# Kernel optimization log

Hardware: AMD Instinct MI355X
Metric: run time of the kernel (lower is better)

The kernel has to match this reference:

```python
import jax, jax.numpy as jnp
import numpy as np
from jax import lax

EPS = 1e-5
SLOPE = 0.2

def knn_idx(x, k):
    # x: [B, C, N] -> neighbor indices [B, N, k] (largest negative sq-dist, self included)
    inner = jnp.einsum('bcn,bcm->bnm', x, x)          # [B,N,N]
    xx = jnp.sum(x * x, axis=1)                        # [B,N]
    pair = 2.0 * inner - xx[:, :, None] - xx[:, None, :]
    return lax.top_k(pair, k)[1]                       # [B,N,k]

def graph_feature(x, idx):
    # x: [B,C,N], idx: [B,N,k] -> edge features [B,N,k,2C] = (x_j - x_i, x_i)
    feat = jnp.transpose(x, (0, 2, 1))                 # [B,N,C]
    nbr = jax.vmap(lambda f, i: f[i])(feat, idx)       # [B,N,k,C]
    ctr = jnp.broadcast_to(feat[:, :, None, :], nbr.shape)
    return jnp.concatenate([nbr - ctr, ctr], axis=-1)  # [B,N,k,2C]

def bn(x, gamma, beta, axes):
    mu = jnp.mean(x, axis=axes, keepdims=True)
    var = jnp.var(x, axis=axes, keepdims=True)
    return (x - mu) * lax.rsqrt(var + EPS) * gamma + beta

def edge_conv(e, w, gamma, beta):
    # e: [B,N,k,2C], w: [O,2C] (1x1 conv, no bias) -> [B,N,O] after BN+LeakyReLU+max over k
    h = jnp.einsum('bnkc,oc->bnko', e, w)
    h = jax.nn.leaky_relu(bn(h, gamma, beta, (0, 1, 2)), SLOPE)
    return jnp.max(h, axis=2)                          # [B,N,O]

def setup_inputs() -> dict:
    key = jax.random.key(0)
    ks = jax.random.split(key, 8)
    B, C, N, O = 8, 3, 4096, 64
    x = jax.random.normal(ks[0], (B, C, N), jnp.float32)
    w_s = jax.random.normal(ks[1], (O, 2 * C), jnp.float32) * (1.0 / np.sqrt(2 * C))
    w_l = jax.random.normal(ks[2], (O, 2 * C), jnp.float32) * (1.0 / np.sqrt(2 * C))
    w_f = jax.random.normal(ks[3], (O, 2 * O), jnp.float32) * (1.0 / np.sqrt(2 * O))
    g_s = jnp.ones((O,)); b_s = jnp.zeros((O,))
    g_l = jnp.ones((O,)); b_l = jnp.zeros((O,))
    g_f = jnp.ones((O,)); b_f = jnp.zeros((O,))
    return {"x": x, "w_s": w_s, "g_s": g_s, "b_s": b_s,
            "w_l": w_l, "g_l": g_l, "b_l": b_l,
            "w_f": w_f, "g_f": g_f, "b_f": b_f}

def reference(x, w_s, g_s, b_s, w_l, g_l, b_l, w_f, g_f, b_f):
    K_SMALL, K_LARGE = 20, 40
    idx_s = knn_idx(x, K_SMALL)
    idx_l = knn_idx(x, K_LARGE)
    h_s = edge_conv(graph_feature(x, idx_s), w_s, g_s, b_s)   # [B,N,O]
    h_l = edge_conv(graph_feature(x, idx_l), w_l, g_l, b_l)   # [B,N,O]
    h = jnp.concatenate([h_s, h_l], axis=-1)                  # [B,N,2O]
    h = jnp.einsum('bnc,oc->bno', h, w_f)                     # fuse 1x1 conv
    h = jax.nn.leaky_relu(bn(h, g_f, b_f, (0, 1)), SLOPE)
    return jnp.transpose(h, (0, 2, 1))                        # [B,O,N]
```

## Files before the change

### kernel.cpp

```cpp
#include <hip/hip_runtime.h>

#define B_ 8
#define N_ 4096
#define O_ 64
#define KL 40
#define KS 20
#define EPSV 1e-5
#define SLOPE 0.2f

typedef unsigned long long u64;
typedef unsigned int u32;

__device__ __forceinline__ float leaky(float v) { return v >= 0.f ? v : SLOPE * v; }

__device__ __forceinline__ u32 mfloat(float x) {
    const u32 u = __float_as_uint(x);
    return (u & 0x80000000u) ? ~u : (u | 0x80000000u);
}
__device__ __forceinline__ float unmfloat(u32 m) {
    return __uint_as_float((m & 0x80000000u) ? (m ^ 0x80000000u) : ~m);
}

template <int S>
__device__ __forceinline__ u64 xor_ex64(u64 v, int dsaddr) {
    if constexpr (S == 1 || S == 2 || S == 8) {
        constexpr int CTRL = (S == 1) ? 0xB1 : (S == 2) ? 0x4E : 0x128;
        const int lo = __builtin_amdgcn_update_dpp(0, (int)(u32)v, CTRL, 0xF, 0xF, true);
        const int hi = __builtin_amdgcn_update_dpp(0, (int)(u32)(v >> 32), CTRL, 0xF, 0xF, true);
        return ((u64)(u32)hi << 32) | (u32)lo;
    } else {
        const int lo = __builtin_amdgcn_ds_bpermute(dsaddr, (int)(u32)v);
        const int hi = __builtin_amdgcn_ds_bpermute(dsaddr, (int)(u32)(v >> 32));
        return ((u64)(u32)hi << 32) | (u32)lo;
    }
}

template <int K, int S>
__device__ __forceinline__ void stage_pair(u64& a, u64& e, int lane, int dsaddr) {
    const u64 oa = xor_ex64<S>(a, dsaddr);
    const u64 oe = xor_ex64<S>(e, dsaddr);
    const bool sel = (((lane & K) == 0) == ((lane & S) == 0));
    a = ((a < oa) == sel) ? a : oa;
    e = ((e < oe) == sel) ? e : oe;
}

__device__ __forceinline__ void sort64_pair(u64& a, u64& e, int lane,
                                            int a4, int a16, int a32) {
    stage_pair<2, 1>(a, e, lane, 0);
    stage_pair<4, 2>(a, e, lane, 0);    stage_pair<4, 1>(a, e, lane, 0);
    stage_pair<8, 4>(a, e, lane, a4);   stage_pair<8, 2>(a, e, lane, 0);    stage_pair<8, 1>(a, e, lane, 0);
    stage_pair<16, 8>(a, e, lane, 0);   stage_pair<16, 4>(a, e, lane, a4);  stage_pair<16, 2>(a, e, lane, 0);   stage_pair<16, 1>(a, e, lane, 0);
    stage_pair<32, 16>(a, e, lane, a16); stage_pair<32, 8>(a, e, lane, 0);  stage_pair<32, 4>(a, e, lane, a4);  stage_pair<32, 2>(a, e, lane, 0);  stage_pair<32, 1>(a, e, lane, 0);
    stage_pair<64, 32>(a, e, lane, a32); stage_pair<64, 16>(a, e, lane, a16); stage_pair<64, 8>(a, e, lane, 0); stage_pair<64, 4>(a, e, lane, a4); stage_pair<64, 2>(a, e, lane, 0); stage_pair<64, 1>(a, e, lane, 0);
}

__device__ __forceinline__ void merge_pair(u64& L0, u64& L1, u64 a, u64 e, int lane,
                                           int a4, int a16, int a32, int a63) {
    const u64 ra = xor_ex64<63>(a, a63);
    const u64 re = xor_ex64<63>(e, a63);
    L0 = (L0 < ra) ? L0 : ra;
    L1 = (L1 < re) ? L1 : re;
    stage_pair<0, 32>(L0, L1, lane, a32);
    stage_pair<0, 16>(L0, L1, lane, a16);
    stage_pair<0, 8>(L0, L1, lane, 0);
    stage_pair<0, 4>(L0, L1, lane, a4);
    stage_pair<0, 2>(L0, L1, lane, 0);
    stage_pair<0, 1>(L0, L1, lane, 0);
}

__global__ __launch_bounds__(1024) void bucket_kernel(const float* __restrict__ x,
                                                      float4* __restrict__ sxp,
                                                      int* __restrict__ perm,
                                                      float2* __restrict__ cb,
                                                      float4* __restrict__ xo4) {
    __shared__ int hist[256];
    __shared__ int ofs[256];
    __shared__ u32 xsm[4096];
    __shared__ float redmin[16], redmax[16];
    __shared__ u32 wmin[64], wmax[64];
    const int b = blockIdx.x;
    const float* xb = x + (size_t)b * 3 * N_;
    const int t = threadIdx.x;
    float xv[4];
    float mn = INFINITY, mx = -INFINITY;
#pragma unroll
    for (int p = 0; p < 4; ++p) {
        xv[p] = xb[t + p * 1024];
        mn = fminf(mn, xv[p]); mx = fmaxf(mx, xv[p]);
    }
#pragma unroll
    for (int s = 1; s < 64; s <<= 1) {
        mn = fminf(mn, __shfl_xor(mn, s));
        mx = fmaxf(mx, __shfl_xor(mx, s));
    }
    if ((t & 63) == 0) { redmin[t >> 6] = mn; redmax[t >> 6] = mx; }
    if (t < 256) hist[t] = 0;
    __syncthreads();
    if (t == 0) {
        float m0 = INFINITY, m1 = -INFINITY;
        for (int w = 0; w < 16; ++w) { m0 = fminf(m0, redmin[w]); m1 = fmaxf(m1, redmax[w]); }
        redmin[0] = m0; redmax[0] = m1;
    }
    __syncthreads();
    const float xmin = redmin[0];
    const float scale = 256.0f / fmaxf(redmax[0] - xmin, 1e-20f);
    int bk[4];
#pragma unroll
    for (int p = 0; p < 4; ++p) {
        bk[p] = min(255, max(0, (int)((xv[p] - xmin) * scale)));
        atomicAdd(&hist[bk[p]], 1);
    }
    __syncthreads();
    if (t == 0) {
        int acc = 0;
        for (int k = 0; k < 256; ++k) { ofs[k] = acc; acc += hist[k]; }
    }
    if (t < 64) { wmin[t] = 0xFFFFFFFFu; wmax[t] = 0; }
    __syncthreads();
#pragma unroll
    for (int p = 0; p < 4; ++p) {
        const int i = t + p * 1024;
        const int dst = atomicAdd(&ofs[bk[p]], 1);
        const float cx = xv[p], cy = xb[N_ + i], cz = xb[2 * N_ + i];
        sxp[((size_t)b << 12) + dst] = make_float4(2.f * cx, 2.f * cy, 2.f * cz,
                                                   -(cx * cx + cy * cy + cz * cz));
        perm[(b << 12) + dst] = i;
        xo4[((size_t)b << 12) + i] = make_float4(cx, cy, cz, 0.f);
        xsm[dst] = mfloat(cx);
    }
    __syncthreads();
#pragma unroll
    for (int p = 0; p < 4; ++p) {
        const int pos = t + p * 1024;
        const int w = pos >> 6;
        atomicMin(&wmin[w], xsm[pos]);
        atomicMax(&wmax[w], xsm[pos]);
    }
    __syncthreads();
    if (t == 0) {
        u32 sm = 0xFFFFFFFFu;
        for (int w = 63; w >= 0; --w) { sm = min(sm, wmin[w]); wmin[w] = sm; }
        u32 pm2 = 0;
        for (int w = 0; w < 64; ++w) { pm2 = max(pm2, wmax[w]); wmax[w] = pm2; }
    }
    __syncthreads();
    if (t < 64) cb[(b << 6) + t] = make_float2(unmfloat(wmin[t]), unmfloat(wmax[t]));
}

__global__ __launch_bounds__(256, 8) void knn_kernel(const float4* __restrict__ sxp,
                                                     const int* __restrict__ perm,
                                                     const float2* __restrict__ cb,
                                                     const float4* __restrict__ xo4,
                                                     const float* __restrict__ w_s,
                                                     const float* __restrict__ w_l,
                                                     float* __restrict__ max_s,
                                                     float* __restrict__ min_s,
                                                     float* __restrict__ max_l,
                                                     float* __restrict__ min_l,
                                                     float* __restrict__ qstats) {
    __shared__ u64 buf[4][2][128];
    __shared__ float2 cbl[64];
    const int sbid = ((blockIdx.x & 7) << 9) | (blockIdx.x >> 3);
    const int b = sbid >> 9;
    const int qbase = (sbid & 511) << 3;
    const int tid = threadIdx.x;
    const int wave = tid >> 6, lane = tid & 63;
    if (tid < 64) cbl[tid] = cb[(b << 6) + tid];
    const int a4 = (lane ^ 4) << 2, a16 = (lane ^ 16) << 2;
    const int a32 = (lane ^ 32) << 2, a63 = (lane ^ 63) << 2;
    const float4* sp = sxp + ((size_t)b << 12);
    const int* pm = perm + (b << 12);
    const float4* xo = xo4 + ((size_t)b << 12);
    const int i0 = qbase + wave * 2;
    const float4 p0 = sp[i0], p1 = sp[i0 + 1];
    const float qx0 = 0.5f * p0.x, qy0 = 0.5f * p0.y, qz0 = 0.5f * p0.z, nw0 = p0.w;
    const float qx1 = 0.5f * p1.x, qy1 = 0.5f * p1.y, qz1 = 0.5f * p1.z, nw1 = p1.w;
    const float qxmin = fminf(qx0, qx1), qxmax = fmaxf(qx0, qx1);
    u64 L0 = ~0ull, L1 = ~0ull;
    float th0 = -INFINITY, th1 = -INFINITY;
    int cnt0 = 0, cnt1 = 0;
    __syncthreads();
    const int home = i0 >> 6;
    int cl = home - 1, cr = home + 1;
    bool openL = (cl >= 0), openR = (cr < 64);
    bool takeR = true;
    int c = home;
    float4 cd = sp[(c << 6) + lane];
    int pj = pm[(c << 6) + lane];
    for (;;) {
        int cn = -1;
        for (;;) {
            if (!openL && !openR) break;
            const bool pickR = openR && (takeR || !openL);
            takeR = !pickR;
            const float r2 = -fminf(th0, th1);
            if (pickR) {
                const float dx = cbl[cr].x - qxmax;
                if (dx > 0.f && dx * dx > r2) { openR = false; continue; }
                cn = cr++; if (cr >= 64) openR = false; break;
            } else {
                const float dx = qxmin - cbl[cl].y;
                if (dx > 0.f && dx * dx > r2) { openL = false; continue; }
                cn = cl--; if (cl < 0) openL = false; break;
            }
        }
        float4 nd = make_float4(0.f, 0.f, 0.f, 0.f);
        int nj = 0;
        if (cn >= 0) { nd = sp[(cn << 6) + lane]; nj = pm[(cn << 6) + lane]; }
        {
            const float d0 = fmaf(qx0, cd.x, fmaf(qy0, cd.y, fmaf(qz0, cd.z, cd.w + nw0)));
            const float d1 = fmaf(qx1, cd.x, fmaf(qy1, cd.y, fmaf(qz1, cd.z, cd.w + nw1)));
            const bool pr0 = (d0 >= th0), pr1 = (d1 >= th1);
            const u64 m0 = __ballot(pr0), m1 = __ballot(pr1);
            if (m0) {
                const int pos = cnt0 + __builtin_amdgcn_mbcnt_hi(
                    (u32)(m0 >> 32), __builtin_amdgcn_mbcnt_lo((u32)m0, 0));
                if (pr0) {
                    const u32 kd = __float_as_uint(fminf(d0, -0.0f));
                    buf[wave][0][pos] = ((u64)kd << 32) | (u32)pj;
                }
                cnt0 += __popcll(m0);
            }
            if (m1) {
                const int pos = cnt1 + __builtin_amdgcn_mbcnt_hi(
                    (u32)(m1 >> 32), __builtin_amdgcn_mbcnt_lo((u32)m1, 0));
                if (pr1) {
                    const u32 kd = __float_as_uint(fminf(d1, -0.0f));
                    buf[wave][1][pos] = ((u64)kd << 32) | (u32)pj;
                }
                cnt1 += __popcll(m1);
            }
            if ((cnt0 | cnt1) >= 64) {
                const int t0 = min(cnt0, 64), t1 = min(cnt1, 64);
                u64 a = (lane < t0) ? buf[wave][0][cnt0 - t0 + lane] : ~0ull;
                u64 e = (lane < t1) ? buf[wave][1][cnt1 - t1 + lane] : ~0ull;
                sort64_pair(a, e, lane, a4, a16, a32);
                merge_pair(L0, L1, a, e, lane, a4, a16, a32, a63);
                th0 = __uint_as_float((u32)__builtin_amdgcn_readlane((int)(u32)(L0 >> 32), KL - 1));
                th1 = __uint_as_float((u32)__builtin_amdgcn_readlane((int)(u32)(L1 >> 32), KL - 1));
                cnt0 -= t0; cnt1 -= t1;
            }
        }
        if (cn < 0) break;
        cd = nd; pj = nj; c = cn;
    }
    if ((cnt0 | cnt1) > 0) {
        u64 a = (lane < cnt0) ? buf[wave][0][lane] : ~0ull;
        u64 e = (lane < cnt1) ? buf[wave][1][lane] : ~0ull;
        sort64_pair(a, e, lane, a4, a16, a32);
        merge_pair(L0, L1, a, e, lane, a4, a16, a32, a63);
    }
    const int lw = lane * 6;
    const float ws0 = w_s[lw], ws1 = w_s[lw + 1], ws2 = w_s[lw + 2];
    const float ds0 = w_s[lw + 3] - ws0, ds1 = w_s[lw + 4] - ws1, ds2 = w_s[lw + 5] - ws2;
    const float wl0 = w_l[lw], wl1 = w_l[lw + 1], wl2 = w_l[lw + 2];
    const float dl0 = w_l[lw + 3] - wl0, dl1 = w_l[lw + 4] - wl1, dl2 = w_l[lw + 5] - wl2;
    const int oi0 = pm[i0], oi1 = pm[i0 + 1];
#pragma unroll
    for (int q = 0; q < 2; ++q) {
        const float qx = q ? qx1 : qx0, qy = q ? qy1 : qy0, qz = q ? qz1 : qz0;
        const int Llo = q ? (int)(u32)L1 : (int)(u32)L0;
        const int oi = q ? oi1 : oi0;
        const float cs = ds0 * qx + ds1 * qy + ds2 * qz;
        const float cq = dl0 * qx + dl1 * qy + dl2 * qz;
        float mxs = -INFINITY, mns = INFINITY, mxl = -INFINITY, mnl = INFINITY;
        float sums = 0.f, sss = 0.f, suml = 0.f, ssl = 0.f;
#pragma unroll 8
        for (int k = 0; k < KL; ++k) {
            const int j = __builtin_amdgcn_readlane(Llo, k);
            const float4 xj = xo[j];
            const float hl = fmaf(wl0, xj.x, fmaf(wl1, xj.y, wl2 * xj.z)) + cq;
            mxl = fmaxf(mxl, hl); mnl = fminf(mnl, hl);
            suml += hl; ssl = fmaf(hl, hl, ssl);
            if (k < KS) {
                const float hs = fmaf(ws0, xj.x, fmaf(ws1, xj.y, ws2 * xj.z)) + cs;
                mxs = fmaxf(mxs, hs); mns = fminf(mns, hs);
                sums += hs; sss = fmaf(hs, hs, sss);
            }
        }
        const size_t base = (size_t)((b << 12) + oi) * 64 + lane;
        max_s[base] = mxs; min_s[base] = mns;
        max_l[base] = mxl; min_l[base] = mnl;
        float* qs = qstats + (size_t)((b << 12) + oi) * 256;
        qs[lane] = sums; qs[64 + lane] = sss;
        qs[128 + lane] = suml; qs[192 + lane] = ssl;
    }
}

__global__ void reduce1a_kernel(const float* __restrict__ qstats, double* __restrict__ partialD1) {
    const int t = threadIdx.x;
    double acc = 0.0;
    const int r0 = blockIdx.x * 256;
    for (int r = 0; r < 256; ++r) acc += (double)qstats[(size_t)(r0 + r) * 256 + t];
    partialD1[(size_t)blockIdx.x * 256 + t] = acc;
}

__global__ void reduce1b_kernel(const double* __restrict__ partialD1,
                                const float* __restrict__ g_s, const float* __restrict__ b_s,
                                const float* __restrict__ g_l, const float* __restrict__ b_l,
                                float* __restrict__ sb1) {
    const int t = threadIdx.x;
    double acc = 0.0;
    for (int r = 0; r < 128; ++r) acc += partialD1[(size_t)r * 256 + t];
    __shared__ double sums[256];
    sums[t] = acc;
    __syncthreads();
    if (t < 64) {
        const double ns = (double)B_ * N_ * KS;
        const double nl = (double)B_ * N_ * KL;
        double mu = sums[t] / ns;
        double var = sums[64 + t] / ns - mu * mu;
        double sc = (double)g_s[t] / sqrt(var + EPSV);
        sb1[t] = (float)sc;
        sb1[64 + t] = (float)((double)b_s[t] - mu * sc);
        mu = sums[128 + t] / nl;
        var = sums[192 + t] / nl - mu * mu;
        sc = (double)g_l[t] / sqrt(var + EPSV);
        sb1[128 + t] = (float)sc;
        sb1[192 + t] = (float)((double)b_l[t] - mu * sc);
    }
}

__global__ __launch_bounds__(256) void fuse_kernel(
    const float* __restrict__ max_s, const float* __restrict__ min_s,
    const float* __restrict__ max_l, const float* __restrict__ min_l,
    const float* __restrict__ sb1, const float* __restrict__ w_f,
    float* __restrict__ f_buf, float* __restrict__ partial2) {
    __shared__ float wfT[128 * 64];
    __shared__ float av[4][128];
    __shared__ float red[2][4][64];
    const int tid = threadIdx.x;
    for (int t = tid; t < 8192; t += 256) {
        const int c = t >> 6, o = t & 63;
        wfT[t] = w_f[o * 128 + c];
    }
    const int sbid = ((blockIdx.x & 7) << 8) + (blockIdx.x >> 3);
    const int wave = tid >> 6, lane = tid & 63;
    const float sc_s = sb1[lane], bi_s = sb1[64 + lane];
    const float sc_l = sb1[128 + lane], bi_l = sb1[192 + lane];
    float sum_f = 0.f, ss_f = 0.f;
    __syncthreads();
    for (int p = 0; p < 4; ++p) {
        const int bn = (sbid * 4 + wave) * 4 + p;
        const size_t base = (size_t)bn * 64 + lane;
        const float hs = sc_s >= 0.f ? max_s[base] : min_s[base];
        const float a_s = leaky(fmaf(sc_s, hs, bi_s));
        const float hl = sc_l >= 0.f ? max_l[base] : min_l[base];
        const float a_l = leaky(fmaf(sc_l, hl, bi_l));
        av[wave][lane] = a_s;
        av[wave][64 + lane] = a_l;
        float acc = 0.f;
#pragma unroll
        for (int c = 0; c < 128; ++c) acc = fmaf(wfT[c * 64 + lane], av[wave][c], acc);
        f_buf[base] = acc;
        sum_f += acc;
        ss_f = fmaf(acc, acc, ss_f);
    }
    red[0][wave][lane] = sum_f;
    red[1][wave][lane] = ss_f;
    __syncthreads();
    if (tid < 128) {
        const int st = tid >> 6, o = tid & 63;
        partial2[(size_t)blockIdx.x * 128 + tid] =
            red[st][0][o] + red[st][1][o] + red[st][2][o] + red[st][3][o];
    }
}

__global__ void reduce2a_kernel(const float* __restrict__ partial2, double* __restrict__ partialD2) {
    const int t = threadIdx.x;
    double acc = 0.0;
    const int r0 = blockIdx.x * 32;
    for (int r = 0; r < 32; ++r) acc += (double)partial2[(size_t)(r0 + r) * 128 + t];
    partialD2[(size_t)blockIdx.x * 128 + t] = acc;
}

__global__ void reduce2b_kernel(const double* __restrict__ partialD2,
                                const float* __restrict__ g_f, const float* __restrict__ b_f,
                                float* __restrict__ sb2) {
    const int t = threadIdx.x;
    double acc = 0.0;
    for (int r = 0; r < 64; ++r) acc += partialD2[(size_t)r * 128 + t];
    __shared__ double sums[128];
    sums[t] = acc;
    __syncthreads();
    if (t < 64) {
        const double n = (double)B_ * N_;
        const double mu = sums[t] / n;
        const double var = sums[64 + t] / n - mu * mu;
        const double sc = (double)g_f[t] / sqrt(var + EPSV);
        sb2[t] = (float)sc;
        sb2[64 + t] = (float)((double)b_f[t] - mu * sc);
    }
}

__global__ __launch_bounds__(256) void final_kernel(const float* __restrict__ f_buf,
                                                    const float* __restrict__ sb2,
                                                    float* __restrict__ out) {
    __shared__ float tile[64][65];
    const int sbid = ((blockIdx.x & 7) << 6) + (blockIdx.x >> 3);
    const int b = sbid >> 6;
    const int n0 = (sbid & 63) << 6;
#pragma unroll
    for (int r = 0; r < 16; ++r) {
        const int t = r * 256 + threadIdx.x;
        const int n = t >> 6, o = t & 63;
        const float v = f_buf[(size_t)((b << 12) + n0 + n) * 64 + o];
        const float h = fmaf(sb2[o], v, sb2[64 + o]);
        tile[n][o] = leaky(h);
    }
    __syncthreads();
#pragma unroll
    for (int r = 0; r < 16; ++r) {
        const int t = r * 256 + threadIdx.x;
        const int o = t >> 6, n = t & 63;
        out[(size_t)((b << 6) + o) * N_ + n0 + n] = tile[n][o];
    }
}

extern "C" void kernel_launch(void* const* d_in, const int* in_sizes, int n_in,
                              void* d_out, int out_size, void* d_ws, size_t ws_size,
                              hipStream_t stream) {
    (void)in_sizes; (void)n_in; (void)out_size; (void)ws_size;
    const float* x   = (const float*)d_in[0];
    const float* w_s = (const float*)d_in[1];
    const float* g_s = (const float*)d_in[2];
    const float* b_s = (const float*)d_in[3];
    const float* w_l = (const float*)d_in[4];
    const float* g_l = (const float*)d_in[5];
    const float* b_l = (const float*)d_in[6];
    const float* w_f = (const float*)d_in[7];
    const float* g_f = (const float*)d_in[8];
    const float* b_f = (const float*)d_in[9];
    float* out = (float*)d_out;
    char* ws = (char*)d_ws;

    constexpr size_t SZ_PT   = (size_t)B_ * N_ * 64 * 4;
    constexpr size_t OFF_MXS = 0;
    constexpr size_t OFF_MNS = OFF_MXS + SZ_PT;
    constexpr size_t OFF_MXL = OFF_MNS + SZ_PT;
    constexpr size_t OFF_MNL = OFF_MXL + SZ_PT;
    constexpr size_t OFF_QST = OFF_MNL + SZ_PT;
    constexpr size_t OFF_PD1 = OFF_QST + (size_t)B_ * N_ * 256 * 4;
    constexpr size_t OFF_SB1 = OFF_PD1 + (size_t)128 * 256 * 8;
    constexpr size_t OFF_F   = OFF_SB1 + 1024;
    constexpr size_t OFF_P2  = OFF_F + SZ_PT;
    constexpr size_t OFF_PD2 = OFF_P2 + (size_t)2048 * 128 * 4;
    constexpr size_t OFF_SB2 = OFF_PD2 + (size_t)64 * 128 * 8;
    constexpr size_t OFF_SXP = OFF_SB2 + 1024;
    constexpr size_t OFF_PRM = OFF_SXP + (size_t)B_ * N_ * 16;
    constexpr size_t OFF_CB  = OFF_PRM + (size_t)B_ * N_ * 4;
    constexpr size_t OFF_XO4 = OFF_CB + (size_t)B_ * 64 * 8;

    float*  mxs  = (float*)(ws + OFF_MXS);
    float*  mns  = (float*)(ws + OFF_MNS);
    float*  mxl  = (float*)(ws + OFF_MXL);
    float*  mnl  = (float*)(ws + OFF_MNL);
    float*  qst  = (float*)(ws + OFF_QST);
    double* pd1  = (double*)(ws + OFF_PD1);
    float*  sb1  = (float*)(ws + OFF_SB1);
    float*  fb   = (float*)(ws + OFF_F);
    float*  p2   = (float*)(ws + OFF_P2);
    double* pd2  = (double*)(ws + OFF_PD2);
    float*  sb2  = (float*)(ws + OFF_SB2);
    float4* sxp  = (float4*)(ws + OFF_SXP);
    int*    prm  = (int*)(ws + OFF_PRM);
    float2* cbv  = (float2*)(ws + OFF_CB);
    float4* xo4  = (float4*)(ws + OFF_XO4);

    hipLaunchKernelGGL(bucket_kernel, dim3(8), dim3(1024), 0, stream, x, sxp, prm, cbv, xo4);
    hipLaunchKernelGGL(knn_kernel, dim3(4096), dim3(256), 0, stream,
                       sxp, prm, cbv, xo4, w_s, w_l, mxs, mns, mxl, mnl, qst);
    hipLaunchKernelGGL(reduce1a_kernel, dim3(128), dim3(256), 0, stream, qst, pd1);
    hipLaunchKernelGGL(reduce1b_kernel, dim3(1), dim3(256), 0, stream, pd1, g_s, b_s, g_l, b_l, sb1);
    hipLaunchKernelGGL(fuse_kernel, dim3(2048), dim3(256), 0, stream,
                       mxs, mns, mxl, mnl, sb1, w_f, fb, p2);
    hipLaunchKernelGGL(reduce2a_kernel, dim3(64), dim3(128), 0, stream, p2, pd2);
    hipLaunchKernelGGL(reduce2b_kernel, dim3(1), dim3(128), 0, stream, pd2, g_f, b_f, sb2);
    hipLaunchKernelGGL(final_kernel, dim3(512), dim3(256), 0, stream, fb, sb2, out);
}
```

Before: 224.7 us.

## Seed kNN list from home chunk, stage neighbor coords in LDS, block-reduce stats

Several changes are combined. The bucket kernel's serial 256-entry prefix sum is replaced with a parallel Hillis-Steele scan. The kNN kernel now seeds its top-k list by sorting the home chunk first, which gives a finite pruning radius before other chunks are visited. It also stages the 40 neighbor coordinates in shared memory instead of issuing per-k readlane gathers from global memory. Per-query BN statistics are summed across the block's waves before being written, cutting qstats traffic and the first reduction by 8x, at the cost of extra shared memory and a block barrier.

Measured after the change: 197.9 us. -11.9%, faster.

```diff
diff --git a/kernel.cpp b/kernel.cpp
--- a/kernel.cpp
+++ b/kernel.cpp
@@ -74,6 +74,7 @@
                                                       float2* __restrict__ cb,
                                                       float4* __restrict__ xo4) {
     __shared__ int hist[256];
+    __shared__ int scan[256];
     __shared__ int ofs[256];
     __shared__ u32 xsm[4096];
     __shared__ float redmin[16], redmax[16];
@@ -111,10 +112,17 @@
         atomicAdd(&hist[bk[p]], 1);
     }
     __syncthreads();
-    if (t == 0) {
-        int acc = 0;
-        for (int k = 0; k < 256; ++k) { ofs[k] = acc; acc += hist[k]; }
-    }
+    if (t < 256) scan[t] = hist[t];
+    __syncthreads();
+#pragma unroll
+    for (int s = 1; s < 256; s <<= 1) {
+        int v = 0;
+        if (t < 256 && t >= s) v = scan[t - s];
+        __syncthreads();
+        if (t < 256) scan[t] += v;
+        __syncthreads();
+    }
+    if (t < 256) ofs[t] = scan[t] - hist[t];
     if (t < 64) { wmin[t] = 0xFFFFFFFFu; wmax[t] = 0; }
     __syncthreads();
 #pragma unroll
@@ -160,6 +168,8 @@
                                                      float* __restrict__ qstats) {
     __shared__ u64 buf[4][2][128];
     __shared__ float2 cbl[64];
+    __shared__ float4 sbuf[4][2][KL];
+    __shared__ float sred[4][4][64];
     const int sbid = ((blockIdx.x & 7) << 9) | (blockIdx.x >> 3);
     const int b = sbid >> 9;
     const int qbase = (sbid & 511) << 3;
@@ -176,18 +186,47 @@
     const float qx0 = 0.5f * p0.x, qy0 = 0.5f * p0.y, qz0 = 0.5f * p0.z, nw0 = p0.w;
     const float qx1 = 0.5f * p1.x, qy1 = 0.5f * p1.y, qz1 = 0.5f * p1.z, nw1 = p1.w;
     const float qxmin = fminf(qx0, qx1), qxmax = fmaxf(qx0, qx1);
-    u64 L0 = ~0ull, L1 = ~0ull;
-    float th0 = -INFINITY, th1 = -INFINITY;
     int cnt0 = 0, cnt1 = 0;
     __syncthreads();
     const int home = i0 >> 6;
+    u64 L0, L1;
+    float th0, th1;
+    {
+        const int js = (home << 6) + lane;
+        const float4 ch = sp[js];
+        const int pj = pm[js];
+        const float d0 = fmaf(qx0, ch.x, fmaf(qy0, ch.y, fmaf(qz0, ch.z, ch.w + nw0)));
+        const float d1 = fmaf(qx1, ch.x, fmaf(qy1, ch.y, fmaf(qz1, ch.z, ch.w + nw1)));
+        u64 k0 = ((u64)__float_as_uint(fminf(d0, -0.0f)) << 32) | (u32)pj;
+        u64 k1 = ((u64)__float_as_uint(fminf(d1, -0.0f)) << 32) | (u32)pj;
+        sort64_pair(k0, k1, lane, a4, a16, a32);
+        L0 = k0; L1 = k1;
+        th0 = __uint_as_float((u32)__builtin_amdgcn_readlane((int)(u32)(L0 >> 32), KL - 1));
+        th1 = __uint_as_float((u32)__builtin_amdgcn_readlane((int)(u32)(L1 >> 32), KL - 1));
+    }
     int cl = home - 1, cr = home + 1;
     bool openL = (cl >= 0), openR = (cr < 64);
     bool takeR = true;
-    int c = home;
-    float4 cd = sp[(c << 6) + lane];
-    int pj = pm[(c << 6) + lane];
+    int c = -1;
+    float4 cd = make_float4(0.f, 0.f, 0.f, 0.f);
+    int pj = 0;
     for (;;) {
+        if (!openL && !openR) break;
+        const bool pickR = openR && (takeR || !openL);
+        takeR = !pickR;
+        const float r2 = -fminf(th0, th1);
+        if (pickR) {
+            const float dx = cbl[cr].x - qxmax;
+            if (dx > 0.f && dx * dx > r2) { openR = false; continue; }
+            c = cr++; if (cr >= 64) openR = false; break;
+        } else {
+            const float dx = qxmin - cbl[cl].y;
+            if (dx > 0.f && dx * dx > r2) { openL = false; continue; }
+            c = cl--; if (cl < 0) openL = false; break;
+        }
+    }
+    if (c >= 0) { cd = sp[(c << 6) + lane]; pj = pm[(c << 6) + lane]; }
+    while (c >= 0) {
         int cn = -1;
         for (;;) {
             if (!openL && !openR) break;
@@ -241,8 +280,7 @@
                 cnt0 -= t0; cnt1 -= t1;
             }
         }
-        if (cn < 0) break;
-        cd = nd; pj = nj; c = cn;
+        c = cn; cd = nd; pj = nj;
     }
     if ((cnt0 | cnt1) > 0) {
         u64 a = (lane < cnt0) ? buf[wave][0][lane] : ~0ull;
@@ -250,30 +288,34 @@
         sort64_pair(a, e, lane, a4, a16, a32);
         merge_pair(L0, L1, a, e, lane, a4, a16, a32, a63);
     }
+    if (lane < KL) {
+        sbuf[wave][0][lane] = xo[(int)((u32)L0 & 4095u)];
+        sbuf[wave][1][lane] = xo[(int)((u32)L1 & 4095u)];
+    }
+    __builtin_amdgcn_wave_barrier();
     const int lw = lane * 6;
     const float ws0 = w_s[lw], ws1 = w_s[lw + 1], ws2 = w_s[lw + 2];
     const float ds0 = w_s[lw + 3] - ws0, ds1 = w_s[lw + 4] - ws1, ds2 = w_s[lw + 5] - ws2;
     const float wl0 = w_l[lw], wl1 = w_l[lw + 1], wl2 = w_l[lw + 2];
     const float dl0 = w_l[lw + 3] - wl0, dl1 = w_l[lw + 4] - wl1, dl2 = w_l[lw + 5] - wl2;
     const int oi0 = pm[i0], oi1 = pm[i0 + 1];
+    float st[4] = {0.f, 0.f, 0.f, 0.f};
 #pragma unroll
     for (int q = 0; q < 2; ++q) {
         const float qx = q ? qx1 : qx0, qy = q ? qy1 : qy0, qz = q ? qz1 : qz0;
-        const int Llo = q ? (int)(u32)L1 : (int)(u32)L0;
         const int oi = q ? oi1 : oi0;
-        const float cs = ds0 * qx + ds1 * qy + ds2 * qz;
-        const float cq = dl0 * qx + dl1 * qy + dl2 * qz;
+        const float cs = fmaf(ds0, qx, fmaf(ds1, qy, ds2 * qz));
+        const float cq = fmaf(dl0, qx, fmaf(dl1, qy, dl2 * qz));
         float mxs = -INFINITY, mns = INFINITY, mxl = -INFINITY, mnl = INFINITY;
         float sums = 0.f, sss = 0.f, suml = 0.f, ssl = 0.f;
-#pragma unroll 8
+#pragma unroll
         for (int k = 0; k < KL; ++k) {
-            const int j = __builtin_amdgcn_readlane(Llo, k);
-            const float4 xj = xo[j];
-            const float hl = fmaf(wl0, xj.x, fmaf(wl1, xj.y, wl2 * xj.z)) + cq;
+            const float4 xj = sbuf[wave][q][k];
+            const float hl = fmaf(wl0, xj.x, fmaf(wl1, xj.y, fmaf(wl2, xj.z, cq)));
             mxl = fmaxf(mxl, hl); mnl = fminf(mnl, hl);
             suml += hl; ssl = fmaf(hl, hl, ssl);
             if (k < KS) {
-                const float hs = fmaf(ws0, xj.x, fmaf(ws1, xj.y, ws2 * xj.z)) + cs;
+                const float hs = fmaf(ws0, xj.x, fmaf(ws1, xj.y, fmaf(ws2, xj.z, cs)));
                 mxs = fmaxf(mxs, hs); mns = fminf(mns, hs);
                 sums += hs; sss = fmaf(hs, hs, sss);
             }
@@ -281,17 +323,23 @@
         const size_t base = (size_t)((b << 12) + oi) * 64 + lane;
         max_s[base] = mxs; min_s[base] = mns;
         max_l[base] = mxl; min_l[base] = mnl;
-        float* qs = qstats + (size_t)((b << 12) + oi) * 256;
-        qs[lane] = sums; qs[64 + lane] = sss;
-        qs[128 + lane] = suml; qs[192 + lane] = ssl;
+        st[0] += sums; st[1] += sss; st[2] += suml; st[3] += ssl;
+    }
+#pragma unroll
+    for (int s = 0; s < 4; ++s) sred[wave][s][lane] = st[s];
+    __syncthreads();
+    if (tid < 256) {
+        const int s = tid >> 6, ch = tid & 63;
+        qstats[(size_t)blockIdx.x * 256 + tid] =
+            sred[0][s][ch] + sred[1][s][ch] + sred[2][s][ch] + sred[3][s][ch];
     }
 }
 
 __global__ void reduce1a_kernel(const float* __restrict__ qstats, double* __restrict__ partialD1) {
     const int t = threadIdx.x;
     double acc = 0.0;
-    const int r0 = blockIdx.x * 256;
-    for (int r = 0; r < 256; ++r) acc += (double)qstats[(size_t)(r0 + r) * 256 + t];
+    const int r0 = blockIdx.x * 128;
+    for (int r = 0; r < 128; ++r) acc += (double)qstats[(size_t)(r0 + r) * 256 + t];
     partialD1[(size_t)blockIdx.x * 256 + t] = acc;
 }
 
@@ -301,7 +349,7 @@
                                 float* __restrict__ sb1) {
     const int t = threadIdx.x;
     double acc = 0.0;
-    for (int r = 0; r < 128; ++r) acc += partialD1[(size_t)r * 256 + t];
+    for (int r = 0; r < 32; ++r) acc += partialD1[(size_t)r * 256 + t];
     __shared__ double sums[256];
     sums[t] = acc;
     __syncthreads();
@@ -440,8 +488,8 @@
     constexpr size_t OFF_MXL = OFF_MNS + SZ_PT;
     constexpr size_t OFF_MNL = OFF_MXL + SZ_PT;
     constexpr size_t OFF_QST = OFF_MNL + SZ_PT;
-    constexpr size_t OFF_PD1 = OFF_QST + (size_t)B_ * N_ * 256 * 4;
-    constexpr size_t OFF_SB1 = OFF_PD1 + (size_t)128 * 256 * 8;
+    constexpr size_t OFF_PD1 = OFF_QST + (size_t)4096 * 256 * 4;
+    constexpr size_t OFF_SB1 = OFF_PD1 + (size_t)32 * 256 * 8;
     constexpr size_t OFF_F   = OFF_SB1 + 1024;
     constexpr size_t OFF_P2  = OFF_F + SZ_PT;
     constexpr size_t OFF_PD2 = OFF_P2 + (size_t)2048 * 128 * 4;
@@ -470,7 +518,7 @@
     hipLaunchKernelGGL(bucket_kernel, dim3(8), dim3(1024), 0, stream, x, sxp, prm, cbv, xo4);
     hipLaunchKernelGGL(knn_kernel, dim3(4096), dim3(256), 0, stream,
                        sxp, prm, cbv, xo4, w_s, w_l, mxs, mns, mxl, mnl, qst);
-    hipLaunchKernelGGL(reduce1a_kernel, dim3(128), dim3(256), 0, stream, qst, pd1);
+    hipLaunchKernelGGL(reduce1a_kernel, dim3(32), dim3(256), 0, stream, qst, pd1);
     hipLaunchKernelGGL(reduce1b_kernel, dim3(1), dim3(256), 0, stream, pd1, g_s, b_s, g_l, b_l, sb1);
     hipLaunchKernelGGL(fuse_kernel, dim3(2048), dim3(256), 0, stream,
                        mxs, mns, mxl, mnl, sb1, w_f, fb, p2);
```
